# Kernel tuning notes

Hardware: AMD Instinct MI355X
Metric: run time of the kernel (lower is better)

## Reference

```python
import jax, jax.numpy as jnp
import numpy as np

STRIDES = (8, 16, 32, 64, 128)
HW = ((100, 128), (50, 64), (25, 32), (13, 16), (7, 8))
NUM_CLASSES = 80
SCORE_THR = 0.05
IOU_THR = 0.6
MAX_NUM = 1000


def _flatten(x):
    # [B,C,H,W] -> [B,H*W,C]  (matches reshape_feats)
    B, C, H, W = x.shape
    return jnp.transpose(x, (0, 2, 3, 1)).reshape(B, H * W, C)


def _coords():
    # center coordinates of every FPN location in input-image scale, concatenated over levels -> [N,2] (x,y)
    cs = []
    for (h, w), s in zip(HW, STRIDES):
        xs = jnp.arange(w, dtype=jnp.float32) * s + s // 2
        ys = jnp.arange(h, dtype=jnp.float32) * s + s // 2
        yy, xx = jnp.meshgrid(ys, xs, indexing='ij')
        cs.append(jnp.stack([xx.reshape(-1), yy.reshape(-1)], axis=-1))
    return jnp.concatenate(cs, axis=0)


def _iou_matrix(boxes):
    # boxes [N,4] (x1,y1,x2,y2) -> pairwise IoU [N,N]
    x1, y1, x2, y2 = jnp.split(boxes, 4, axis=-1)  # each [N,1]
    area = jnp.clip(x2 - x1, 0.0) * jnp.clip(y2 - y1, 0.0)
    ix1 = jnp.maximum(x1, x1.T)
    iy1 = jnp.maximum(y1, y1.T)
    ix2 = jnp.minimum(x2, x2.T)
    iy2 = jnp.minimum(y2, y2.T)
    inter = jnp.clip(ix2 - ix1, 0.0) * jnp.clip(iy2 - iy1, 0.0)
    union = area + area.T - inter
    return inter / jnp.maximum(union, 1e-9)


def _nms_single(scores, labels, boxes):
    # Per-image class-aware greedy NMS on topk candidates; returns fixed-size padded
    # (scores, labels, boxes, keep_mask) where suppressed/below-thr entries have keep=False.
    valid = scores > SCORE_THR  # score_mask from _post_process
    s = jnp.where(valid, scores, -1.0)
    order = jnp.argsort(-s)
    s = s[order]
    lb = labels[order]
    bx = boxes[order]
    valid = valid[order]
    # class-offset trick from _batch_nms: offset boxes per label by (coord_max + 1)
    coord_max = jnp.max(jnp.where(valid[:, None], bx, 0.0))
    off = lb.astype(bx.dtype) * (coord_max + 1.0)
    iou = _iou_matrix(bx + off[:, None])
    N = s.shape[0]
    idx = jnp.arange(N)

    def body(i, keep):
        sup = keep[i] & (iou[i] > IOU_THR) & (idx > i)
        return keep & jnp.logical_not(sup)

    keep = jax.lax.fori_loop(0, N, body, valid)
    return jnp.where(keep, s, 0.0), jnp.where(keep, lb, 0), bx, keep


def setup_inputs() -> dict:
    key = jax.random.key(0)
    ks = jax.random.split(key, 15)
    inp = {}
    i = 0
    for name, c, scale in (('cls', NUM_CLASSES, None), ('reg', 4, 128.0), ('ctr', 1, None)):
        for lvl, (h, w) in zip((3, 4, 5, 6, 7), HW):
            if scale is None:
                x = jax.random.normal(ks[i], (16, c, h, w), dtype=jnp.float32)
            else:
                x = jax.random.uniform(ks[i], (16, c, h, w), dtype=jnp.float32) * scale
            inp[f'{name}_p{lvl}'] = x
            i += 1
    return inp


def reference(cls_p3, cls_p4, cls_p5, cls_p6, cls_p7,
              reg_p3, reg_p4, reg_p5, reg_p6, reg_p7,
              ctr_p3, ctr_p4, ctr_p5, ctr_p6, ctr_p7):
    cls = jnp.concatenate([_flatten(t) for t in (cls_p3, cls_p4, cls_p5, cls_p6, cls_p7)], axis=1)  # [B,N,80]
    reg = jnp.concatenate([_flatten(t) for t in (reg_p3, reg_p4, reg_p5, reg_p6, reg_p7)], axis=1)  # [B,N,4]
    ctr = jnp.concatenate([_flatten(t) for t in (ctr_p3, ctr_p4, ctr_p5, ctr_p6, ctr_p7)], axis=1)  # [B,N,1]

    cls_preds = jax.nn.sigmoid(cls)
    ctr_preds = jax.nn.sigmoid(ctr)[..., 0]
    cls_scores = jnp.max(cls_preds, axis=-1)
    pred_labels = jnp.argmax(cls_preds, axis=-1) + 1  # labels start at 1
    cls_scores = jnp.sqrt(cls_scores * ctr_preds)  # use_ctr=True fusion

    coords = _coords()  # [N,2]
    pred_boxes = jnp.concatenate([coords - reg[..., :2], coords + reg[..., 2:]], axis=-1)  # [B,N,4]

    topk_s, topk_i = jax.lax.top_k(cls_scores, MAX_NUM)
    topk_l = jnp.take_along_axis(pred_labels, topk_i, axis=1)
    topk_b = jnp.take_along_axis(pred_boxes, topk_i[..., None], axis=1)

    return jax.vmap(_nms_single)(topk_s, topk_l, topk_b)
```

## Files before the change

kernel.cpp:

```cpp
#include <hip/hip_runtime.h>
#include <cstdint>


typedef unsigned long long ull;

#define BATCH 16
#define NLOC 17064
#define NPAD 18432
#define NCHUNK 9
#define CHUNK 2048
#define TOPK 1000
#define TOPKP 1024
#define NCLS 80
#define SCORE_THR 0.05f
#define IOU_THR 0.6f

struct Ptrs { const float* cls[5]; const float* reg[5]; const float* ctr[5]; };

__global__ __launch_bounds__(256) void score_kernel(Ptrs p, ull* __restrict__ keys,
                                                    int* __restrict__ labels,
                                                    float* __restrict__ boxes) {
  int idx = blockIdx.x * 256 + threadIdx.x;
  if (idx >= BATCH * NPAD) return;
  int b = idx / NPAD, n = idx - b * NPAD;
  if (n >= NLOC) { keys[idx] = 0ull; return; }

  int lvl, off, lw, st, H;
  if (n < 12800)      { lvl=0; off=0;     lw=7; st=8;   H=100; }
  else if (n < 16000) { lvl=1; off=12800; lw=6; st=16;  H=50;  }
  else if (n < 16800) { lvl=2; off=16000; lw=5; st=32;  H=25;  }
  else if (n < 17008) { lvl=3; off=16800; lw=4; st=64;  H=13;  }
  else                { lvl=4; off=17008; lw=3; st=128; H=7;   }
  int hw = n - off;
  int w = hw & ((1 << lw) - 1), h = hw >> lw;
  int HW = H << lw;
  float fs = (float)st, half = fs * 0.5f;
  float x = (float)w * fs + half, y = (float)h * fs + half;

  const float* cb = p.cls[lvl] + (size_t)b * NCLS * HW + hw;
  float best = cb[0]; int bi = 0;
  for (int c = 1; c < NCLS; ++c) {
    float v = cb[(size_t)c * HW];
    if (v > best) { best = v; bi = c; }
  }
  const float* rb = p.reg[lvl] + (size_t)b * 4 * HW + hw;
  float r0 = rb[0], r1 = rb[HW], r2 = rb[2 * (size_t)HW], r3 = rb[3 * (size_t)HW];
  float ct = p.ctr[lvl][(size_t)b * HW + hw];

  float pcls = 1.f / (1.f + expf(-best));
  float pctr = 1.f / (1.f + expf(-ct));
  float score = sqrtf(pcls * pctr);

  keys[idx] = ((ull)__float_as_uint(score) << 32) | (ull)(0xFFFFFFFFu - (unsigned)n);
  labels[(size_t)b * NLOC + n] = bi + 1;
  float* bx = boxes + ((size_t)b * NLOC + n) * 4;
  bx[0] = x - r0; bx[1] = y - r1; bx[2] = x + r2; bx[3] = y + r3;
}

__global__ __launch_bounds__(512) void chunk_sort_kernel(const ull* __restrict__ keys,
                                                         ull* __restrict__ runs) {
  __shared__ ull s[CHUNK];
  int b = blockIdx.x / NCHUNK, c = blockIdx.x % NCHUNK;
  const ull* src = keys + (size_t)b * NPAD + (size_t)c * CHUNK;
  for (int i = threadIdx.x; i < CHUNK; i += 512) s[i] = src[i];
  __syncthreads();
  for (int k = 2; k <= CHUNK; k <<= 1) {
    for (int j = k >> 1; j > 0; j >>= 1) {
      for (int t = threadIdx.x; t < CHUNK / 2; t += 512) {
        int i = ((t & ~(j - 1)) << 1) | (t & (j - 1));
        int ixj = i | j;
        bool desc = (i & k) == 0;
        ull a = s[i], bb = s[ixj];
        bool sw = desc ? (a < bb) : (a > bb);
        if (sw) { s[i] = bb; s[ixj] = a; }
      }
      __syncthreads();
    }
  }
  ull* dst = runs + ((size_t)b * NCHUNK + c) * TOPKP;
  for (int i = threadIdx.x; i < TOPKP; i += 512) dst[i] = s[i];
}

__global__ __launch_bounds__(512) void merge_level_kernel(const ull* __restrict__ src,
    ull* __restrict__ dst, int npairs, int carry, int srcRPI, int dstRPI) {
  int per = npairs + carry;
  int b = blockIdx.x / per, p = blockIdx.x % per;
  const ull* sb = src + (size_t)b * srcRPI * TOPKP;
  ull* db = dst + (size_t)b * dstRPI * TOPKP;
  int tid = threadIdx.x;
  if (p >= npairs) {
    for (int i = tid; i < TOPKP; i += 512)
      db[(size_t)p * TOPKP + i] = sb[(size_t)(2 * npairs) * TOPKP + i];
    return;
  }
  __shared__ ull m[TOPKP];
  const ull* A = sb + (size_t)(2 * p) * TOPKP;
  const ull* B = sb + (size_t)(2 * p + 1) * TOPKP;
  for (int i = tid; i < TOPKP; i += 512) {
    ull a = A[i], c = B[TOPKP - 1 - i];
    m[i] = a > c ? a : c;
  }
  __syncthreads();
  for (int j = TOPKP / 2; j > 0; j >>= 1) {
    for (int t = tid; t < TOPKP / 2; t += 512) {
      int i = ((t & ~(j - 1)) << 1) | (t & (j - 1));
      int ixj = i | j;
      ull a = m[i], c = m[ixj];
      if (a < c) { m[i] = c; m[ixj] = a; }
    }
    __syncthreads();
  }
  for (int i = tid; i < TOPKP; i += 512) db[(size_t)p * TOPKP + i] = m[i];
}

__global__ __launch_bounds__(256) void gather_kernel(const ull* __restrict__ topkeys,
    const int* __restrict__ labels, const float* __restrict__ boxes,
    float* __restrict__ topS, int* __restrict__ topL, float* __restrict__ topOB,
    ull* __restrict__ validWords, float* __restrict__ outBoxes) {
  __shared__ float red[256];
  __shared__ float s_cmax;
  int b = blockIdx.x, tid = threadIdx.x;
  float lmax = 0.f;
  for (int k = tid; k < TOPKP; k += 256) {
    ull key = topkeys[(size_t)b * TOPKP + k];
    float sc = 0.f; int lb = 0;
    float b0 = 0.f, b1 = 0.f, b2 = 0.f, b3 = 0.f;
    bool inR = (k < TOPK);
    if (inR) {
      sc = __uint_as_float((unsigned)(key >> 32));
      unsigned n = 0xFFFFFFFFu - (unsigned)(key & 0xFFFFFFFFull);
      lb = labels[(size_t)b * NLOC + n];
      const float* bp = boxes + ((size_t)b * NLOC + n) * 4;
      b0 = bp[0]; b1 = bp[1]; b2 = bp[2]; b3 = bp[3];
      float* ob = outBoxes + ((size_t)b * TOPK + k) * 4;
      ob[0] = b0; ob[1] = b1; ob[2] = b2; ob[3] = b3;
    }
    topS[(size_t)b * TOPKP + k] = sc;
    topL[(size_t)b * TOPKP + k] = lb;
    float* tb = topOB + ((size_t)b * TOPKP + k) * 4;
    tb[0] = b0; tb[1] = b1; tb[2] = b2; tb[3] = b3;
    bool valid = inR && (sc > SCORE_THR);
    if (valid) lmax = fmaxf(lmax, fmaxf(fmaxf(b0, b1), fmaxf(b2, b3)));
    ull vb = __ballot(valid ? 1 : 0);
    if ((tid & 63) == 0) validWords[b * 16 + (k >> 6)] = vb;
  }
  red[tid] = lmax;
  __syncthreads();
  for (int sft = 128; sft > 0; sft >>= 1) {
    if (tid < sft) red[tid] = fmaxf(red[tid], red[tid + sft]);
    __syncthreads();
  }
  if (tid == 0) s_cmax = red[0];
  __syncthreads();
  float offb = s_cmax + 1.0f;
  for (int k = tid; k < TOPKP; k += 256) {
    float off = (float)topL[(size_t)b * TOPKP + k] * offb;
    float* tb = topOB + ((size_t)b * TOPKP + k) * 4;
    tb[0] += off; tb[1] += off; tb[2] += off; tb[3] += off;
  }
}

__global__ __launch_bounds__(1024) void sup_kernel(const float* __restrict__ topOB,
                                                   ull* __restrict__ sup) {
  int bid = blockIdx.x;
  int b = bid / TOPK, i = bid - b * TOPK;
  int j = threadIdx.x;
  const float4* OB = (const float4*)topOB + (size_t)b * TOPKP;
  float4 A = OB[i];
  float aw = fmaxf(A.z - A.x, 0.f), ah = fmaxf(A.w - A.y, 0.f);
  float areaA = aw * ah;
  bool bit = false;
  if (j > i && j < TOPK) {
    float4 Bx = OB[j];
    float bw = fmaxf(Bx.z - Bx.x, 0.f), bh = fmaxf(Bx.w - Bx.y, 0.f);
    float areaB = bw * bh;
    float ix1 = fmaxf(A.x, Bx.x), iy1 = fmaxf(A.y, Bx.y);
    float ix2 = fminf(A.z, Bx.z), iy2 = fminf(A.w, Bx.w);
    float inter = fmaxf(ix2 - ix1, 0.f) * fmaxf(iy2 - iy1, 0.f);
    float uni = areaA + areaB - inter;
    float iou = inter / fmaxf(uni, 1e-9f);
    bit = iou > IOU_THR;
  }
  ull m = __ballot(bit ? 1 : 0);
  if ((j & 63) == 0) sup[((size_t)b * TOPKP + i) * 16 + (j >> 6)] = m;
}

__global__ __launch_bounds__(256) void nms_scan_kernel(const ull* __restrict__ sup,
    const ull* __restrict__ validWords, const float* __restrict__ topS,
    const int* __restrict__ topL, float* __restrict__ out) {
  __shared__ ull ls[2][2048];
  int b = blockIdx.x, tid = threadIdx.x;
  int wave = tid >> 6, lane = tid & 63;
  const ull* S = sup + (size_t)b * TOPKP * 16;

  ull rm = 0xFFFFFFFFFFFFFFFFull;
  if (wave == 0 && lane < 16) rm = ~validWords[b * 16 + lane];

  {
    ull s0 = S[tid], s1 = S[tid + 256], s2 = S[tid + 512], s3 = S[tid + 768],
        s4 = S[tid + 1024], s5 = S[tid + 1280], s6 = S[tid + 1536],
        s7 = S[tid + 1792];
    ls[0][tid] = s0;        ls[0][tid + 256] = s1;  ls[0][tid + 512] = s2;
    ls[0][tid + 768] = s3;  ls[0][tid + 1024] = s4; ls[0][tid + 1280] = s5;
    ls[0][tid + 1536] = s6; ls[0][tid + 1792] = s7;
  }
  __syncthreads();

  for (int g = 0; g < 8; ++g) {
    ull s0 = 0, s1 = 0, s2 = 0, s3 = 0, s4 = 0, s5 = 0, s6 = 0, s7 = 0;
    bool st = (g < 7);
    if (st) {
      const ull* src = S + (size_t)(g + 1) * 2048;
      s0 = src[tid];        s1 = src[tid + 256];  s2 = src[tid + 512];
      s3 = src[tid + 768];  s4 = src[tid + 1024]; s5 = src[tid + 1280];
      s6 = src[tid + 1536]; s7 = src[tid + 1792];
    }
    __builtin_amdgcn_sched_barrier(0);

    if (wave == 0) {
      const ull* Bf = ls[g & 1];
      int lg = lane >> 4, wd = lane & 15;
      for (int wl = 0; wl < 2; ++wl) {
        int w = 2 * g + wl;
        ull dg = Bf[(size_t)(wl * 64 + lane) * 16 + w];
        unsigned dlo = (unsigned)dg, dhi = (unsigned)(dg >> 32);
        unsigned mlo = __builtin_amdgcn_readlane((unsigned)rm, w);
        unsigned mhi = __builtin_amdgcn_readlane((unsigned)(rm >> 32), w);
        ull M = ~(((ull)mhi << 32) | (ull)mlo);
        ull nz = __ballot(dg != 0ull);
        ull R = ~M;
        ull cand;
        while ((cand = nz & ~R) != 0ull) {
          int k = (int)__builtin_ctzll(cand);
          unsigned rl = __builtin_amdgcn_readlane(dlo, k);
          unsigned rh = __builtin_amdgcn_readlane(dhi, k);
          R |= (((ull)rh << 32) | (ull)rl);
          nz &= ~(1ull << k);
        }
        ull km = ~R;
        const ull* RB = Bf + (size_t)(wl * 64 + lg) * 16 + wd;
        ull accB = 0;
#pragma unroll
        for (int t = 0; t < 16; ++t) {
          ull bit = (km >> (4 * t + lg)) & 1ull;
          accB |= RB[(size_t)t * 64] & (0ull - bit);
        }
        accB |= __shfl_xor(accB, 16);
        accB |= __shfl_xor(accB, 32);
        rm |= accB;
      }
    }

    if (st) {
      ull* dst = ls[(g + 1) & 1];
      dst[tid] = s0;        dst[tid + 256] = s1;  dst[tid + 512] = s2;
      dst[tid + 768] = s3;  dst[tid + 1024] = s4; dst[tid + 1280] = s5;
      dst[tid + 1536] = s6; dst[tid + 1792] = s7;
    }
    __syncthreads();
  }

  if (wave == 0) {
    ull keep_na = ~rm;
    const float* tS = topS + (size_t)b * TOPKP;
    const int*   tL = topL + (size_t)b * TOPKP;
    float* outS = out;
    float* outL = out + BATCH * TOPK;
    float* outK = out + BATCH * TOPK * 6;
    for (int t = 0; t < 16; ++t) {
      int j = t * 64 + lane;
      ull kw = __shfl(keep_na, t);
      if (j < TOPK) {
        bool kp = (kw >> lane) & 1ull;
        outS[(size_t)b * TOPK + j] = kp ? tS[j] : 0.f;
        outL[(size_t)b * TOPK + j] = kp ? (float)tL[j] : 0.f;
        outK[(size_t)b * TOPK + j] = kp ? 1.f : 0.f;
      }
    }
  }
}

extern "C" void kernel_launch(void* const* d_in, const int* in_sizes, int n_in,
                              void* d_out, int out_size, void* d_ws, size_t ws_size,
                              hipStream_t stream) {
  Ptrs p;
  for (int l = 0; l < 5; ++l) {
    p.cls[l] = (const float*)d_in[l];
    p.reg[l] = (const float*)d_in[5 + l];
    p.ctr[l] = (const float*)d_in[10 + l];
  }
  char* ws = (char*)d_ws;
  size_t o = 0;
  auto alloc = [&](size_t bytes) -> void* {
    void* r = ws + o; o += (bytes + 255) & ~(size_t)255; return r;
  };
  ull*   keys       = (ull*)  alloc((size_t)BATCH * NPAD * 8);
  int*   labels     = (int*)  alloc((size_t)BATCH * NLOC * 4);
  float* boxes      = (float*)alloc((size_t)BATCH * NLOC * 16);
  ull*   runs       = (ull*)  alloc((size_t)BATCH * NCHUNK * TOPKP * 8);
  ull*   runs2      = (ull*)  alloc((size_t)BATCH * NCHUNK * TOPKP * 8);
  ull*   topkeys    = (ull*)  alloc((size_t)BATCH * TOPKP * 8);
  float* topS       = (float*)alloc((size_t)BATCH * TOPKP * 4);
  int*   topL       = (int*)  alloc((size_t)BATCH * TOPKP * 4);
  float* topOB      = (float*)alloc((size_t)BATCH * TOPKP * 16);
  ull*   validWords = (ull*)  alloc((size_t)BATCH * 16 * 8);
  ull*   sup        = (ull*)  alloc((size_t)BATCH * TOPKP * 16 * 8);

  float* out = (float*)d_out;
  float* outBoxes = out + 2 * BATCH * TOPK;

  hipLaunchKernelGGL(score_kernel, dim3((BATCH * NPAD + 255) / 256), dim3(256), 0, stream,
                     p, keys, labels, boxes);
  hipLaunchKernelGGL(chunk_sort_kernel, dim3(BATCH * NCHUNK), dim3(512), 0, stream,
                     keys, runs);
  hipLaunchKernelGGL(merge_level_kernel, dim3(BATCH * 5), dim3(512), 0, stream,
                     runs, runs2, 4, 1, NCHUNK, NCHUNK);
  hipLaunchKernelGGL(merge_level_kernel, dim3(BATCH * 3), dim3(512), 0, stream,
                     runs2, runs, 2, 1, NCHUNK, NCHUNK);
  hipLaunchKernelGGL(merge_level_kernel, dim3(BATCH * 2), dim3(512), 0, stream,
                     runs, runs2, 1, 1, NCHUNK, NCHUNK);
  hipLaunchKernelGGL(merge_level_kernel, dim3(BATCH * 1), dim3(512), 0, stream,
                     runs2, topkeys, 1, 0, NCHUNK, 1);
  hipLaunchKernelGGL(gather_kernel, dim3(BATCH), dim3(256), 0, stream,
                     topkeys, labels, boxes, topS, topL, topOB, validWords, outBoxes);
  hipLaunchKernelGGL(sup_kernel, dim3(BATCH * TOPK), dim3(1024), 0, stream,
                     topOB, sup);
  hipLaunchKernelGGL(nms_scan_kernel, dim3(BATCH), dim3(256), 0, stream,
                     sup, validWords, topS, topL, out);
}
```

Measured before the change: 231.1 us.

## Fuse tree merge levels and gather into one sequential per-image merge kernel

```diff
diff --git a/kernel.cpp b/kernel.cpp
--- a/kernel.cpp
+++ b/kernel.cpp
@@ -81,48 +81,40 @@
   for (int i = threadIdx.x; i < TOPKP; i += 512) dst[i] = s[i];
 }
 
-__global__ __launch_bounds__(512) void merge_level_kernel(const ull* __restrict__ src,
-    ull* __restrict__ dst, int npairs, int carry, int srcRPI, int dstRPI) {
-  int per = npairs + carry;
-  int b = blockIdx.x / per, p = blockIdx.x % per;
-  const ull* sb = src + (size_t)b * srcRPI * TOPKP;
-  ull* db = dst + (size_t)b * dstRPI * TOPKP;
-  int tid = threadIdx.x;
-  if (p >= npairs) {
-    for (int i = tid; i < TOPKP; i += 512)
-      db[(size_t)p * TOPKP + i] = sb[(size_t)(2 * npairs) * TOPKP + i];
-    return;
-  }
+__global__ __launch_bounds__(512) void merge_gather_kernel(
+    const ull* __restrict__ runs, const int* __restrict__ labels,
+    const float* __restrict__ boxes, float* __restrict__ topS,
+    int* __restrict__ topL, float* __restrict__ topOB,
+    ull* __restrict__ validWords, float* __restrict__ outBoxes) {
   __shared__ ull m[TOPKP];
-  const ull* A = sb + (size_t)(2 * p) * TOPKP;
-  const ull* B = sb + (size_t)(2 * p + 1) * TOPKP;
-  for (int i = tid; i < TOPKP; i += 512) {
-    ull a = A[i], c = B[TOPKP - 1 - i];
-    m[i] = a > c ? a : c;
-  }
-  __syncthreads();
-  for (int j = TOPKP / 2; j > 0; j >>= 1) {
-    for (int t = tid; t < TOPKP / 2; t += 512) {
-      int i = ((t & ~(j - 1)) << 1) | (t & (j - 1));
-      int ixj = i | j;
-      ull a = m[i], c = m[ixj];
-      if (a < c) { m[i] = c; m[ixj] = a; }
-    }
-    __syncthreads();
-  }
-  for (int i = tid; i < TOPKP; i += 512) db[(size_t)p * TOPKP + i] = m[i];
-}
-
-__global__ __launch_bounds__(256) void gather_kernel(const ull* __restrict__ topkeys,
-    const int* __restrict__ labels, const float* __restrict__ boxes,
-    float* __restrict__ topS, int* __restrict__ topL, float* __restrict__ topOB,
-    ull* __restrict__ validWords, float* __restrict__ outBoxes) {
-  __shared__ float red[256];
+  __shared__ float red[512];
   __shared__ float s_cmax;
   int b = blockIdx.x, tid = threadIdx.x;
+  const ull* rbase = runs + (size_t)b * NCHUNK * TOPKP;
+
+  for (int i = tid; i < TOPKP; i += 512) m[i] = rbase[i];
+  __syncthreads();
+  for (int r = 1; r < NCHUNK; ++r) {
+    const ull* B = rbase + (size_t)r * TOPKP;
+    for (int i = tid; i < TOPKP; i += 512) {
+      ull a = m[i], c = B[TOPKP - 1 - i];
+      if (c > a) m[i] = c;
+    }
+    __syncthreads();
+    for (int j = TOPKP / 2; j > 0; j >>= 1) {
+      for (int t = tid; t < TOPKP / 2; t += 512) {
+        int i = ((t & ~(j - 1)) << 1) | (t & (j - 1));
+        int ixj = i | j;
+        ull a = m[i], c = m[ixj];
+        if (a < c) { m[i] = c; m[ixj] = a; }
+      }
+      __syncthreads();
+    }
+  }
+
   float lmax = 0.f;
-  for (int k = tid; k < TOPKP; k += 256) {
-    ull key = topkeys[(size_t)b * TOPKP + k];
+  for (int k = tid; k < TOPKP; k += 512) {
+    ull key = m[k];
     float sc = 0.f; int lb = 0;
     float b0 = 0.f, b1 = 0.f, b2 = 0.f, b3 = 0.f;
     bool inR = (k < TOPK);
@@ -146,14 +138,14 @@
   }
   red[tid] = lmax;
   __syncthreads();
-  for (int sft = 128; sft > 0; sft >>= 1) {
+  for (int sft = 256; sft > 0; sft >>= 1) {
     if (tid < sft) red[tid] = fmaxf(red[tid], red[tid + sft]);
     __syncthreads();
   }
   if (tid == 0) s_cmax = red[0];
   __syncthreads();
   float offb = s_cmax + 1.0f;
-  for (int k = tid; k < TOPKP; k += 256) {
+  for (int k = tid; k < TOPKP; k += 512) {
     float off = (float)topL[(size_t)b * TOPKP + k] * offb;
     float* tb = topOB + ((size_t)b * TOPKP + k) * 4;
     tb[0] += off; tb[1] += off; tb[2] += off; tb[3] += off;
@@ -298,8 +290,6 @@
   int*   labels     = (int*)  alloc((size_t)BATCH * NLOC * 4);
   float* boxes      = (float*)alloc((size_t)BATCH * NLOC * 16);
   ull*   runs       = (ull*)  alloc((size_t)BATCH * NCHUNK * TOPKP * 8);
-  ull*   runs2      = (ull*)  alloc((size_t)BATCH * NCHUNK * TOPKP * 8);
-  ull*   topkeys    = (ull*)  alloc((size_t)BATCH * TOPKP * 8);
   float* topS       = (float*)alloc((size_t)BATCH * TOPKP * 4);
   int*   topL       = (int*)  alloc((size_t)BATCH * TOPKP * 4);
   float* topOB      = (float*)alloc((size_t)BATCH * TOPKP * 16);
@@ -313,16 +303,8 @@
                      p, keys, labels, boxes);
   hipLaunchKernelGGL(chunk_sort_kernel, dim3(BATCH * NCHUNK), dim3(512), 0, stream,
                      keys, runs);
-  hipLaunchKernelGGL(merge_level_kernel, dim3(BATCH * 5), dim3(512), 0, stream,
-                     runs, runs2, 4, 1, NCHUNK, NCHUNK);
-  hipLaunchKernelGGL(merge_level_kernel, dim3(BATCH * 3), dim3(512), 0, stream,
-                     runs2, runs, 2, 1, NCHUNK, NCHUNK);
-  hipLaunchKernelGGL(merge_level_kernel, dim3(BATCH * 2), dim3(512), 0, stream,
-                     runs, runs2, 1, 1, NCHUNK, NCHUNK);
-  hipLaunchKernelGGL(merge_level_kernel, dim3(BATCH * 1), dim3(512), 0, stream,
-                     runs2, topkeys, 1, 0, NCHUNK, 1);
-  hipLaunchKernelGGL(gather_kernel, dim3(BATCH), dim3(256), 0, stream,
-                     topkeys, labels, boxes, topS, topL, topOB, validWords, outBoxes);
+  hipLaunchKernelGGL(merge_gather_kernel, dim3(BATCH), dim3(512), 0, stream,
+                     runs, labels, boxes, topS, topL, topOB, validWords, outBoxes);
   hipLaunchKernelGGL(sup_kernel, dim3(BATCH * TOPK), dim3(1024), 0, stream,
                      topOB, sup);
   hipLaunchKernelGGL(nms_scan_kernel, dim3(BATCH), dim3(256), 0, stream,
```

Result: no change. 229.5 us (-0.7%).
